# Kernel optimization log

Measured on AMD Instinct MI355X. Metric: run time of the kernel, lower is better.

Reference implementation:

```python
import jax, jax.numpy as jnp
import numpy as np

HIDDEN = 1024
Q_OUT = 2048
KV_OUT = 1024
HEAD_DIM = 128
N_Q = Q_OUT // HEAD_DIM      # 16
N_KV = KV_OUT // HEAD_DIM    # 8
EPS = 1e-6
ROPE_BASE = 10000.0


def _rms_norm(x, w, eps=EPS):
    # normalize over last dim (head_dim)
    ms = jnp.mean(x * x, axis=-1, keepdims=True)
    return x * jax.lax.rsqrt(ms + eps) * w


def _rope_cos_sin(t, dim=HEAD_DIM, base=ROPE_BASE):
    inv_freq = 1.0 / (base ** (jnp.arange(0, dim, 2, dtype=jnp.float32) / dim))
    pos = jnp.arange(t, dtype=jnp.float32)
    freqs = pos[:, None] * inv_freq[None, :]          # (T, D/2)
    emb = jnp.concatenate([freqs, freqs], axis=-1)    # (T, D)
    return jnp.cos(emb), jnp.sin(emb)


def _rotate_half(x):
    d = x.shape[-1] // 2
    return jnp.concatenate([-x[..., d:], x[..., :d]], axis=-1)


def setup_inputs() -> dict:
    key = jax.random.key(0)
    ks = jax.random.split(key, 7)
    def lin(k, fan_in, fan_out):
        # nn.Linear default init: U(-1/sqrt(fan_in), 1/sqrt(fan_in)); stored as (in, out) for x @ W
        bound = 1.0 / np.sqrt(fan_in)
        return jax.random.uniform(k, (fan_in, fan_out), jnp.float32, -bound, bound)
    return {
        "x": jax.random.normal(ks[0], (2, 2048, HIDDEN), jnp.float32),
        "Wq": lin(ks[1], HIDDEN, Q_OUT),
        "Wk": lin(ks[2], HIDDEN, KV_OUT),
        "Wv": lin(ks[3], HIDDEN, KV_OUT),
        "Wo": lin(ks[4], Q_OUT, HIDDEN),
        "q_norm_w": jnp.ones((HEAD_DIM,), jnp.float32),
        "k_norm_w": jnp.ones((HEAD_DIM,), jnp.float32),
    }


def reference(x, Wq, Wk, Wv, Wo, q_norm_w, k_norm_w):
    b, t, _ = x.shape
    # QKV projections, shaped to (B, H, T, D)
    q = (x @ Wq).reshape(b, t, N_Q, HEAD_DIM).transpose(0, 2, 1, 3)
    k = (x @ Wk).reshape(b, t, N_KV, HEAD_DIM).transpose(0, 2, 1, 3)
    v = (x @ Wv).reshape(b, t, N_KV, HEAD_DIM).transpose(0, 2, 1, 3)
    # per-head RMSNorm on q/k
    q = _rms_norm(q, q_norm_w)
    k = _rms_norm(k, k_norm_w)
    # RoPE (positions 0..T-1)
    cos, sin = _rope_cos_sin(t)                        # (T, D)
    cos = cos[None, None]; sin = sin[None, None]       # (1,1,T,D)
    q = q * cos + _rotate_half(q) * sin
    k = k * cos + _rotate_half(k) * sin
    # GQA: repeat_interleave kv heads to match q heads
    rep = N_Q // N_KV
    k_r = jnp.repeat(k, rep, axis=1)                   # (B, Hq, T, D)
    v_r = jnp.repeat(v, rep, axis=1)
    # causal attention
    scores = jnp.einsum('bhqd,bhkd->bhqk', q, k_r) / jnp.sqrt(jnp.asarray(HEAD_DIM, x.dtype))
    causal = jnp.triu(jnp.full((t, t), -jnp.inf, dtype=scores.dtype), k=1)[None, None]
    attn = jax.nn.softmax(scores + causal, axis=-1)
    out = jnp.einsum('bhqk,bhkd->bhqd', attn, v_r)     # (B, Hq, T, D)
    out = out.transpose(0, 2, 1, 3).reshape(b, t, Q_OUT)
    return out @ Wo
```

## Files before the change

### kernel.cpp

```cpp
#include <hip/hip_runtime.h>
#include <math.h>

typedef __attribute__((ext_vector_type(8))) short short8;
typedef __attribute__((ext_vector_type(4))) float f32x4;
typedef __attribute__((ext_vector_type(4))) unsigned int uint4v;

#define HIDDEN 1024
#define QOUT 2048
#define KVOUT 1024
#define HD 128
#define TSEQ 2048

__device__ __forceinline__ float bf2f(unsigned short h) {
    union { unsigned int u; float f; } x; x.u = ((unsigned int)h) << 16; return x.f;
}
__device__ __forceinline__ unsigned short f2bf(float f) {
    union { float f; unsigned int u; } x; x.f = f;
    unsigned int r = (x.u + 0x7fffu + ((x.u >> 16) & 1u)) >> 16;
    return (unsigned short)r;
}
__device__ __forceinline__ unsigned int cvtpk(float lo, float hi) {
    unsigned int r;
    asm("v_cvt_pk_bf16_f32 %0, %1, %2" : "=v"(r) : "v"(lo), "v"(hi));
    return r;
}
__device__ __forceinline__ void pl32(unsigned int& a, unsigned int& b) {
    asm("v_permlane32_swap_b32 %0, %1" : "+v"(a), "+v"(b));
}
__device__ __forceinline__ void pl16(unsigned int& a, unsigned int& b) {
    asm("v_permlane16_swap_b32 %0, %1" : "+v"(a), "+v"(b));
}

__device__ __forceinline__ void glds16(const unsigned short* g, unsigned short* l) {
    __builtin_amdgcn_global_load_lds(
        (const __attribute__((address_space(1))) unsigned int*)g,
        (__attribute__((address_space(3))) unsigned int*)l, 16, 0, 0);
}

__global__ __launch_bounds__(256) void prep(const float* __restrict__ x,
                                            const float* __restrict__ Wq,
                                            const float* __restrict__ Wk,
                                            const float* __restrict__ Wv,
                                            const float* __restrict__ Wo,
                                            unsigned short* __restrict__ xb,
                                            unsigned short* __restrict__ Wt,
                                            unsigned short* __restrict__ Wot) {
    int bid = blockIdx.x;
    int tid = threadIdx.x;
    if (bid < 4096) {
        int i = bid * 256 + tid;
        float4 v = *(const float4*)(x + (size_t)i * 4);
        unsigned short o[4] = {f2bf(v.x), f2bf(v.y), f2bf(v.z), f2bf(v.w)};
        *(unsigned long long*)(xb + (size_t)i * 4) = *(unsigned long long*)o;
        return;
    }
    bid -= 4096;
    const float* W; unsigned short* D; int K, N;
    if (bid < 512)       { W = Wq; D = Wt;                          K = 1024; N = 2048; }
    else if (bid < 768)  { bid -= 512;  W = Wk; D = Wt + (size_t)2048 * 1024; K = 1024; N = 1024; }
    else if (bid < 1024) { bid -= 768;  W = Wv; D = Wt + (size_t)3072 * 1024; K = 1024; N = 1024; }
    else                 { bid -= 1024; W = Wo; D = Wot;                      K = 2048; N = 1024; }
    __shared__ __attribute__((aligned(16))) unsigned short Ls[64 * 72];
    int ntiles = N >> 6;
    int kt = bid / ntiles, nt = bid - kt * ntiles;
    int k0 = kt * 64, n0 = nt * 64;
    for (int t = 0; t < 4; t++) {
        int idx = tid + t * 256;
        int r = idx >> 4, seg = idx & 15;
        float4 v = *(const float4*)(W + (size_t)(k0 + r) * N + n0 + seg * 4);
        int c = seg * 4;
        Ls[(c + 0) * 72 + r] = f2bf(v.x);
        Ls[(c + 1) * 72 + r] = f2bf(v.y);
        Ls[(c + 2) * 72 + r] = f2bf(v.z);
        Ls[(c + 3) * 72 + r] = f2bf(v.w);
    }
    __syncthreads();
    for (int t = 0; t < 2; t++) {
        int idx = tid + t * 256;
        int rr = idx >> 3, seg = idx & 7;
        uint4v v = *(const uint4v*)(Ls + rr * 72 + seg * 8);
        *(uint4v*)(D + (size_t)(n0 + rr) * K + k0 + seg * 8) = v;
    }
}

template <int OUT_BF16, int BN>
__global__ __launch_bounds__(256) void gemm_bt(const unsigned short* __restrict__ A,
                                               const unsigned short* __restrict__ Bt,
                                               void* __restrict__ Cout,
                                               int M, int N, int K) {
    constexpr int MT = (BN == 128) ? 4 : 2;
    __shared__ __attribute__((aligned(16))) unsigned short As[2][128 * 32];
    __shared__ __attribute__((aligned(16))) unsigned short Bs[2][BN * 32];
    const int tid = threadIdx.x;
    const int lane = tid & 63;
    const int warp = tid >> 6;
    const int ln = lane & 15;
    const int quad = lane >> 4;
    const int wm = (BN == 128) ? (warp >> 1) : warp;
    const int wn = (BN == 128) ? (warp & 1) : 0;
    const int m0 = blockIdx.y * 128;
    const int n0 = blockIdx.x * BN;

    const int srow = lane >> 2;
    const int schunk = (lane & 3) ^ (srow & 3);
    const unsigned short* Ag = A + (size_t)(m0 + warp * 16 + srow) * K + schunk * 8;
    const unsigned short* Bg = Bt + (size_t)(n0 + warp * 16 + srow) * K + schunk * 8;

    f32x4 acc[MT][4];
#pragma unroll
    for (int i = 0; i < MT; i++)
#pragma unroll
        for (int j = 0; j < 4; j++) acc[i][j] = (f32x4){0.f, 0.f, 0.f, 0.f};

    auto stage = [&](int k0, int bi) {
        glds16(Ag + k0, As[bi] + warp * 16 * 32);
        glds16(Ag + (size_t)64 * K + k0, As[bi] + warp * 16 * 32 + 64 * 32);
        glds16(Bg + k0, Bs[bi] + warp * 16 * 32);
        if (BN == 128) glds16(Bg + (size_t)64 * K + k0, Bs[bi] + warp * 16 * 32 + 64 * 32);
    };

    const int rq = quad ^ (ln & 3);
    const int KI = K >> 5;
    stage(0, 0);
    for (int it = 0; it < KI; it++) {
        __syncthreads();
        if (it + 1 < KI) stage((it + 1) << 5, (it + 1) & 1);
        const unsigned short* Ab = As[it & 1];
        const unsigned short* Bb = Bs[it & 1];
        short8 af[MT], bf[4];
#pragma unroll
        for (int mt = 0; mt < MT; mt++)
            af[mt] = *(const short8*)(Ab + (wm * (MT * 16) + mt * 16 + ln) * 32 + rq * 8);
#pragma unroll
        for (int nt = 0; nt < 4; nt++)
            bf[nt] = *(const short8*)(Bb + (wn * 64 + nt * 16 + ln) * 32 + rq * 8);
#pragma unroll
        for (int mt = 0; mt < MT; mt++)
#pragma unroll
            for (int nt = 0; nt < 4; nt++)
                acc[mt][nt] = __builtin_amdgcn_mfma_f32_16x16x32_bf16(bf[nt], af[mt], acc[mt][nt], 0, 0, 0);
    }
#pragma unroll
    for (int mt = 0; mt < MT; mt++) {
        int row = m0 + wm * (MT * 16) + mt * 16 + ln;
#pragma unroll
        for (int nt = 0; nt < 4; nt++) {
            int colb = n0 + wn * 64 + nt * 16 + quad * 4;
            if (OUT_BF16) {
                unsigned long long pk =
                    (unsigned long long)cvtpk(acc[mt][nt][0], acc[mt][nt][1]) |
                    ((unsigned long long)cvtpk(acc[mt][nt][2], acc[mt][nt][3]) << 32);
                *(unsigned long long*)((unsigned short*)Cout + (size_t)row * N + colb) = pk;
            } else {
                *(f32x4*)((float*)Cout + (size_t)row * N + colb) = acc[mt][nt];
            }
        }
    }
}

template <int OUT_BF16>
__global__ __launch_bounds__(256) void gemm_o(const unsigned short* __restrict__ A,
                                              const unsigned short* __restrict__ Bt,
                                              void* __restrict__ Cout,
                                              int M, int N, int K) {
    __shared__ __attribute__((aligned(16))) unsigned short As[2][128 * 64];
    __shared__ __attribute__((aligned(16))) unsigned short Bs[2][64 * 64];
    const int tid = threadIdx.x;
    const int lane = tid & 63;
    const int warp = tid >> 6;
    const int ln = lane & 15;
    const int quad = lane >> 4;
    const int m0 = blockIdx.y * 128;
    const int n0 = blockIdx.x * 64;

    const int srow = lane >> 3;
    const int schunk = (lane & 7) ^ srow;
    const unsigned short* Ag = A + (size_t)(m0 + warp * 32 + srow) * K + schunk * 8;
    const unsigned short* Bg = Bt + (size_t)(n0 + warp * 16 + srow) * K + schunk * 8;

    f32x4 acc[2][4];
#pragma unroll
    for (int i = 0; i < 2; i++)
#pragma unroll
        for (int j = 0; j < 4; j++) acc[i][j] = (f32x4){0.f, 0.f, 0.f, 0.f};

    auto stage = [&](int k0, int bi) {
#pragma unroll
        for (int g = 0; g < 4; g++)
            glds16(Ag + (size_t)(g * 8) * K + k0, As[bi] + (warp * 32 + g * 8) * 64);
#pragma unroll
        for (int g = 0; g < 2; g++)
            glds16(Bg + (size_t)(g * 8) * K + k0, Bs[bi] + (warp * 16 + g * 8) * 64);
    };

    const int KI = K >> 6;
    stage(0, 0);
    for (int it = 0; it < KI; it++) {
        __syncthreads();
        if (it + 1 < KI) stage((it + 1) << 6, (it + 1) & 1);
        const unsigned short* Ab = As[it & 1];
        const unsigned short* Bb = Bs[it & 1];
#pragma unroll
        for (int ks = 0; ks < 2; ks++) {
            const int rc = ((ks << 2) + quad) ^ (ln & 7);
            short8 af[2], bf[4];
#pragma unroll
            for (int mt = 0; mt < 2; mt++)
                af[mt] = *(const short8*)(Ab + (warp * 32 + mt * 16 + ln) * 64 + rc * 8);
#pragma unroll
            for (int nt = 0; nt < 4; nt++)
                bf[nt] = *(const short8*)(Bb + (nt * 16 + ln) * 64 + rc * 8);
#pragma unroll
            for (int mt = 0; mt < 2; mt++)
#pragma unroll
                for (int nt = 0; nt < 4; nt++)
                    acc[mt][nt] = __builtin_amdgcn_mfma_f32_16x16x32_bf16(bf[nt], af[mt], acc[mt][nt], 0, 0, 0);
        }
    }
#pragma unroll
    for (int mt = 0; mt < 2; mt++) {
        int row = m0 + warp * 32 + mt * 16 + ln;
#pragma unroll
        for (int nt = 0; nt < 4; nt++) {
            int colb = n0 + nt * 16 + quad * 4;
            if (OUT_BF16) {
                unsigned long long pk =
                    (unsigned long long)cvtpk(acc[mt][nt][0], acc[mt][nt][1]) |
                    ((unsigned long long)cvtpk(acc[mt][nt][2], acc[mt][nt][3]) << 32);
                *(unsigned long long*)((unsigned short*)Cout + (size_t)row * N + colb) = pk;
            } else {
                *(f32x4*)((float*)Cout + (size_t)row * N + colb) = acc[mt][nt];
            }
        }
    }
}

__global__ __launch_bounds__(256) void nrvt(const unsigned short* __restrict__ QKV,
                                            const float* __restrict__ qw,
                                            const float* __restrict__ kw,
                                            unsigned short* __restrict__ Q,
                                            unsigned short* __restrict__ Kb,
                                            unsigned short* __restrict__ Vt) {
    if (blockIdx.x < 12288) {
        const int tid = threadIdx.x;
        const int l5 = tid & 31;
        const int task = blockIdx.x * 8 + (tid >> 5);
        const int tok = task / 24;
        const int slot = task - tok * 24;
        const int b = tok >> 11, t = tok & 2047;
        const float* w;
        unsigned short* dst;
        int col0;
        float sc;
        if (slot < 16) {
            col0 = slot * HD;
            dst = Q + ((size_t)(b * 16 + slot) * TSEQ + t) * HD;
            w = qw;
            sc = 0.12750580997495268f;
        } else {
            int hk = slot - 16;
            col0 = QOUT + hk * HD;
            dst = Kb + ((size_t)(b * 8 + hk) * TSEQ + t) * HD;
            w = kw;
            sc = 1.0f;
        }
        const unsigned short* row = QKV + (size_t)tok * 4096 + col0;
        unsigned long long pkin = *(const unsigned long long*)(row + l5 * 4);
        unsigned short us[4];
        *(unsigned long long*)us = pkin;
        float e[4];
        float ss = 0.f;
#pragma unroll
        for (int k = 0; k < 4; k++) { e[k] = bf2f(us[k]); ss += e[k] * e[k]; }
#pragma unroll
        for (int off = 1; off < 32; off <<= 1) ss += __shfl_xor(ss, off);
        float rr = rsqrtf(ss * (1.0f / 128.0f) + 1e-6f);
        float4 wv = *(const float4*)(w + l5 * 4);
        float n[4] = { e[0] * rr * wv.x, e[1] * rr * wv.y, e[2] * rr * wv.z, e[3] * rr * wv.w };
        float np[4];
#pragma unroll
        for (int k = 0; k < 4; k++) np[k] = __shfl_xor(n[k], 16);
        const float tf = (float)t;
        const int fb = (l5 & 15) * 4;
        const bool hi = (l5 >= 16);
        unsigned short outs[4];
#pragma unroll
        for (int k = 0; k < 4; k++) {
            float invf = __builtin_exp2f(-(float)(fb + k) * 0.20762050593045951f);
            float sf, cf;
            __sincosf(tf * invf, &sf, &cf);
            float o = hi ? (n[k] * cf + np[k] * sf) : (n[k] * cf - np[k] * sf);
            outs[k] = f2bf(o * sc);
        }
        *(unsigned long long*)(dst + l5 * 4) = *(unsigned long long*)outs;
        return;
    }
    __shared__ __attribute__((aligned(16))) unsigned short Ls[128 * 72];
    int bid = blockIdx.x - 12288;
    int tt = bid & 31, hk = (bid >> 5) & 7, b = bid >> 8;
    int t0 = tt * 64;
    int tid = threadIdx.x;
    const unsigned short* base = QKV + (size_t)(b * 2048 + t0) * 4096 + 3072 + hk * 128;
    for (int i = 0; i < 4; i++) {
        int idx = tid + i * 256;
        int r = idx >> 4, seg = idx & 15;
        uint4v v = *(const uint4v*)(base + (size_t)r * 4096 + seg * 8);
        unsigned short* pv = (unsigned short*)&v;
        int d = seg * 8;
        for (int jj = 0; jj < 8; jj++) Ls[(d + jj) * 72 + r] = pv[jj];
    }
    __syncthreads();
    unsigned short* out = Vt + (size_t)(b * 8 + hk) * 128 * 2048;
    for (int i = 0; i < 4; i++) {
        int idx = tid + i * 256;
        int d = idx >> 3, seg = idx & 7;
        uint4v v = *(const uint4v*)(Ls + d * 72 + seg * 8);
        *(uint4v*)(out + (size_t)d * 2048 + t0 + seg * 8) = v;
    }
}

__global__ __launch_bounds__(512, 4) void attn(const unsigned short* __restrict__ Q,
                                               const unsigned short* __restrict__ Kg,
                                               const unsigned short* __restrict__ Vt,
                                               unsigned short* __restrict__ Og) {
    __shared__ __attribute__((aligned(16))) unsigned short Ks[2][64 * 128];
    __shared__ __attribute__((aligned(16))) unsigned short Vs[2][128 * 64];
    const int p = blockIdx.x;
    const int bh = blockIdx.y;
    const int b = bh >> 4, h = bh & 15, hk = h >> 1;
    const int tid = threadIdx.x;
    const int w = tid >> 6, lane = tid & 63, ln = lane & 15, quad = lane >> 4;
    const int sg = w >> 2;
    const int wi = w & 3;
    const int tile = sg ? (31 - p) : p;
    const int jdiag = tile;
    const int qrow0 = tile * 64 + wi * 16;

    const unsigned short* Kbase = Kg + (size_t)(b * 8 + hk) * TSEQ * HD;
    const unsigned short* Vbase = Vt + (size_t)(b * 8 + hk) * HD * TSEQ;
    const unsigned short* Qh = Q + (size_t)(b * 16 + h) * TSEQ * HD;

    short8 qf[4];
#pragma unroll
    for (int kt = 0; kt < 4; kt++)
        qf[kt] = *(const short8*)(Qh + (size_t)(qrow0 + ln) * HD + kt * 32 + quad * 8);

    f32x4 o[8];
    f32x4 lac = (f32x4){0.f, 0.f, 0.f, 0.f};
#pragma unroll
    for (int ot = 0; ot < 8; ot++) o[ot] = (f32x4){0.f, 0.f, 0.f, 0.f};
    float m_ = -1e30f;

    const int kr = lane >> 4;
    const int kc = lane & 15;
    const int vr = lane >> 3;
    const int vc = lane & 7;

    auto stage_kv = [&](int jt, int bi) {
        const int j0s = jt * 64;
        unsigned short* KsB = Ks[bi];
        unsigned short* VsB = Vs[bi];
#pragma unroll
        for (int c = 0; c < 2; c++) {
            int row = w * 8 + c * 4 + kr;
            glds16(Kbase + (size_t)(j0s + row) * HD + ((kc ^ (row & 15)) * 8),
                   KsB + (w * 8 + c * 4) * 128);
        }
#pragma unroll
        for (int c = 0; c < 2; c++) {
            int d = w * 16 + c * 8 + vr;
            glds16(Vbase + (size_t)d * TSEQ + j0s + ((vc ^ (d & 7)) * 8),
                   VsB + (w * 16 + c * 8) * 64);
        }
    };

    short8 ones8;
#pragma unroll
    for (int i = 0; i < 8; i++) ones8[i] = (short)0x3F80;

    const int nT = 32 - p;
    stage_kv(0, 0);
    for (int j = 0; j < nT; j++) {
        __syncthreads();
        if (j + 1 < nT) stage_kv(j + 1, (j + 1) & 1);
        const unsigned short* KsC = Ks[j & 1];
        const unsigned short* VsC = Vs[j & 1];
        const bool act = sg ? true : (j <= jdiag);
        if (act) {
            f32x4 s[4];
#pragma unroll
            for (int kb = 0; kb < 4; kb++) s[kb] = (f32x4){0.f, 0.f, 0.f, 0.f};
            __builtin_amdgcn_s_setprio(1);
#pragma unroll
            for (int kt = 0; kt < 4; kt++) {
                short8 kf[4];
#pragma unroll
                for (int kb = 0; kb < 4; kb++)
                    kf[kb] = *(const short8*)(KsC + (kb * 16 + ln) * 128 + (((kt * 4 + quad) ^ ln) * 8));
#pragma unroll
                for (int kb = 0; kb < 4; kb++)
                    s[kb] = __builtin_amdgcn_mfma_f32_16x16x32_bf16(kf[kb], qf[kt], s[kb], 0, 0, 0);
            }
            __builtin_amdgcn_s_setprio(0);
            float mk[4];
            if (j == jdiag) {
                const int qloc = wi * 16 + ln;
#pragma unroll
                for (int kb = 0; kb < 4; kb++) {
#pragma unroll
                    for (int r = 0; r < 4; r++) {
                        int kvloc = kb * 16 + quad * 4 + r;
                        if (kvloc > qloc) s[kb][r] = -1e30f;
                    }
                    mk[kb] = fmaxf(fmaxf(s[kb][0], s[kb][1]), fmaxf(s[kb][2], s[kb][3]));
                }
            } else {
#pragma unroll
                for (int kb = 0; kb < 4; kb++)
                    mk[kb] = fmaxf(fmaxf(s[kb][0], s[kb][1]), fmaxf(s[kb][2], s[kb][3]));
            }
            float mx = fmaxf(fmaxf(mk[0], mk[1]), fmaxf(mk[2], mk[3]));
            float mn = m_;
            bool needR = false;
            float alpha = 1.f;
            if (!__all(mx <= mn + 8.0f)) {
                mx = fmaxf(mx, __shfl_xor(mx, 16));
                mx = fmaxf(mx, __shfl_xor(mx, 32));
                mn = fmaxf(m_, mx);
                alpha = __builtin_exp2f(m_ - mn);
                m_ = mn;
                needR = true;
            }
            unsigned int u[8];
#pragma unroll
            for (int kb = 0; kb < 4; kb++) {
                float p0 = __builtin_exp2f(s[kb][0] - mn);
                float p1 = __builtin_exp2f(s[kb][1] - mn);
                float p2 = __builtin_exp2f(s[kb][2] - mn);
                float p3 = __builtin_exp2f(s[kb][3] - mn);
                u[kb * 2 + 0] = cvtpk(p0, p1);
                u[kb * 2 + 1] = cvtpk(p2, p3);
            }
            pl32(u[0], u[2]); pl16(u[0], u[2]);
            pl32(u[1], u[3]); pl16(u[1], u[3]);
            pl32(u[4], u[6]); pl16(u[4], u[6]);
            pl32(u[5], u[7]); pl16(u[5], u[7]);
            union { unsigned int uu[4]; short8 s8; } P0, P1;
            P0.uu[0] = u[0]; P0.uu[1] = u[1]; P0.uu[2] = u[2]; P0.uu[3] = u[3];
            P1.uu[0] = u[4]; P1.uu[1] = u[5]; P1.uu[2] = u[6]; P1.uu[3] = u[7];
            short8 pf0 = P0.s8;
            short8 pf1 = P1.s8;
            if (needR) {
#pragma unroll
                for (int ot = 0; ot < 8; ot++)
#pragma unroll
                    for (int r = 0; r < 4; r++) o[ot][r] *= alpha;
#pragma unroll
                for (int r = 0; r < 4; r++) lac[r] *= alpha;
            }
            __builtin_amdgcn_s_setprio(1);
            lac = __builtin_amdgcn_mfma_f32_16x16x32_bf16(ones8, pf0, lac, 0, 0, 0);
            lac = __builtin_amdgcn_mfma_f32_16x16x32_bf16(ones8, pf1, lac, 0, 0, 0);
#pragma unroll
            for (int ot = 0; ot < 8; ot++) {
                short8 vf0 = *(const short8*)(VsC + (ot * 16 + ln) * 64 + ((quad ^ (ln & 7)) * 8));
                short8 vf1 = *(const short8*)(VsC + (ot * 16 + ln) * 64 + (((4 + quad) ^ (ln & 7)) * 8));
                o[ot] = __builtin_amdgcn_mfma_f32_16x16x32_bf16(vf0, pf0, o[ot], 0, 0, 0);
                o[ot] = __builtin_amdgcn_mfma_f32_16x16x32_bf16(vf1, pf1, o[ot], 0, 0, 0);
            }
            __builtin_amdgcn_s_setprio(0);
        }
    }
    float inv = 1.0f / lac[0];
    size_t rowoff = ((size_t)(b * TSEQ + qrow0 + ln)) * QOUT + h * 128 + quad * 4;
#pragma unroll
    for (int ot = 0; ot < 8; ot++) {
        unsigned long long pk =
            (unsigned long long)cvtpk(o[ot][0] * inv, o[ot][1] * inv) |
            ((unsigned long long)cvtpk(o[ot][2] * inv, o[ot][3] * inv) << 32);
        *(unsigned long long*)(Og + rowoff + ot * 16) = pk;
    }
}

extern "C" void kernel_launch(void* const* d_in, const int* in_sizes, int n_in,
                              void* d_out, int out_size, void* d_ws, size_t ws_size,
                              hipStream_t stream) {
    (void)in_sizes; (void)n_in; (void)out_size;
    const float* x  = (const float*)d_in[0];
    const float* Wq = (const float*)d_in[1];
    const float* Wk = (const float*)d_in[2];
    const float* Wv = (const float*)d_in[3];
    const float* Wo = (const float*)d_in[4];
    const float* qw = (const float*)d_in[5];
    const float* kw = (const float*)d_in[6];

    char* ws = (char*)d_ws;
    const size_t MB = 1024 * 1024;
    unsigned short* Wt   = (unsigned short*)(ws);
    unsigned short* Wot  = (unsigned short*)(ws + 8 * MB);
    unsigned short* QKVb = (unsigned short*)(ws + 12 * MB);
    unsigned short* xb   = (unsigned short*)(ws + 44 * MB);
    unsigned short* Qb   = (unsigned short*)(ws + 52 * MB);
    unsigned short* Kb   = (unsigned short*)(ws + 68 * MB);
    unsigned short* Vtb  = (unsigned short*)(ws + 76 * MB);
    unsigned short* Ob   = (unsigned short*)(ws + 84 * MB);
    if (ws_size < 100 * MB) return;

    prep<<<dim3(5632), 256, 0, stream>>>(x, Wq, Wk, Wv, Wo, xb, Wt, Wot);
    gemm_bt<1, 128><<<dim3(32, 32), 256, 0, stream>>>(xb, Wt, QKVb, 4096, 4096, 1024);
    nrvt<<<dim3(12800), 256, 0, stream>>>(QKVb, qw, kw, Qb, Kb, Vtb);
    attn<<<dim3(16, 32), 512, 0, stream>>>(Qb, Kb, Vtb, Ob);
    gemm_o<0><<<dim3(16, 32), 256, 0, stream>>>(Ob, Wot, (float*)d_out, 4096, 1024, 2048);
}
```

Before: 251.3 us.

## Halve attention KV tile to 32 keys and double occupancy bound

Shrinks the per-iteration KV tile in the flash-attention kernel from 64 to 32 keys, halving LDS use, and raises launch bounds from 4 to 8 blocks per CU. The V tile gets a new packed layout with two head-dim rows per LDS row, and the causal diagonal is tracked per 32-key half-tile, so warps skip more fully masked work. The intent is more resident blocks and finer causal skipping. The cost is twice as many barriers and staging rounds per query tile, and tighter register limits that could cause spills.

```diff
diff --git a/kernel.cpp b/kernel.cpp
--- a/kernel.cpp
+++ b/kernel.cpp
@@ -319,12 +319,12 @@
     }
 }
 
-__global__ __launch_bounds__(512, 4) void attn(const unsigned short* __restrict__ Q,
+__global__ __launch_bounds__(512, 8) void attn(const unsigned short* __restrict__ Q,
                                                const unsigned short* __restrict__ Kg,
                                                const unsigned short* __restrict__ Vt,
                                                unsigned short* __restrict__ Og) {
-    __shared__ __attribute__((aligned(16))) unsigned short Ks[2][64 * 128];
-    __shared__ __attribute__((aligned(16))) unsigned short Vs[2][128 * 64];
+    __shared__ __attribute__((aligned(16))) unsigned short Ks[2][32 * 128];
+    __shared__ __attribute__((aligned(16))) unsigned short Vs[2][64 * 64];
     const int p = blockIdx.x;
     const int bh = blockIdx.y;
     const int b = bh >> 4, h = bh & 15, hk = h >> 1;
@@ -333,7 +333,7 @@
     const int sg = w >> 2;
     const int wi = w & 3;
     const int tile = sg ? (31 - p) : p;
-    const int jdiag = tile;
+    const int jdiag = 2 * tile + (wi >> 1);
     const int qrow0 = tile * 64 + wi * 16;
 
     const unsigned short* Kbase = Kg + (size_t)(b * 8 + hk) * TSEQ * HD;
@@ -351,26 +351,19 @@
     for (int ot = 0; ot < 8; ot++) o[ot] = (f32x4){0.f, 0.f, 0.f, 0.f};
     float m_ = -1e30f;
 
-    const int kr = lane >> 4;
-    const int kc = lane & 15;
-    const int vr = lane >> 3;
-    const int vc = lane & 7;
-
     auto stage_kv = [&](int jt, int bi) {
-        const int j0s = jt * 64;
-        unsigned short* KsB = Ks[bi];
-        unsigned short* VsB = Vs[bi];
-#pragma unroll
-        for (int c = 0; c < 2; c++) {
-            int row = w * 8 + c * 4 + kr;
-            glds16(Kbase + (size_t)(j0s + row) * HD + ((kc ^ (row & 15)) * 8),
-                   KsB + (w * 8 + c * 4) * 128);
-        }
-#pragma unroll
-        for (int c = 0; c < 2; c++) {
-            int d = w * 16 + c * 8 + vr;
-            glds16(Vbase + (size_t)d * TSEQ + j0s + ((vc ^ (d & 7)) * 8),
-                   VsB + (w * 16 + c * 8) * 64);
+        const int j0s = jt * 32;
+        {
+            int row = w * 4 + (lane >> 4);
+            int kchunk = lane & 15;
+            glds16(Kbase + (size_t)(j0s + row) * HD + ((kchunk ^ (row & 15)) * 8),
+                   Ks[bi] + (w * 4) * 128);
+        }
+        {
+            int r = w * 8 + (lane >> 3);
+            int c = (lane & 7) ^ (r & 7);
+            glds16(Vbase + (size_t)(2 * r + (c >> 2)) * TSEQ + j0s + (c & 3) * 8,
+                   Vs[bi] + (w * 8) * 64);
         }
     };
 
@@ -378,48 +371,42 @@
 #pragma unroll
     for (int i = 0; i < 8; i++) ones8[i] = (short)0x3F80;
 
-    const int nT = 32 - p;
+    const int nT = 64 - 2 * p;
     stage_kv(0, 0);
     for (int j = 0; j < nT; j++) {
         __syncthreads();
         if (j + 1 < nT) stage_kv(j + 1, (j + 1) & 1);
         const unsigned short* KsC = Ks[j & 1];
         const unsigned short* VsC = Vs[j & 1];
-        const bool act = sg ? true : (j <= jdiag);
-        if (act) {
-            f32x4 s[4];
-#pragma unroll
-            for (int kb = 0; kb < 4; kb++) s[kb] = (f32x4){0.f, 0.f, 0.f, 0.f};
+        if (j <= jdiag) {
+            f32x4 s[2];
+            s[0] = (f32x4){0.f, 0.f, 0.f, 0.f};
+            s[1] = (f32x4){0.f, 0.f, 0.f, 0.f};
             __builtin_amdgcn_s_setprio(1);
 #pragma unroll
             for (int kt = 0; kt < 4; kt++) {
-                short8 kf[4];
-#pragma unroll
-                for (int kb = 0; kb < 4; kb++)
+                short8 kf[2];
+#pragma unroll
+                for (int kb = 0; kb < 2; kb++)
                     kf[kb] = *(const short8*)(KsC + (kb * 16 + ln) * 128 + (((kt * 4 + quad) ^ ln) * 8));
 #pragma unroll
-                for (int kb = 0; kb < 4; kb++)
+                for (int kb = 0; kb < 2; kb++)
                     s[kb] = __builtin_amdgcn_mfma_f32_16x16x32_bf16(kf[kb], qf[kt], s[kb], 0, 0, 0);
             }
             __builtin_amdgcn_s_setprio(0);
-            float mk[4];
             if (j == jdiag) {
-                const int qloc = wi * 16 + ln;
-#pragma unroll
-                for (int kb = 0; kb < 4; kb++) {
+                const int qrel = wi * 16 + ln - ((wi >> 1) << 5);
+#pragma unroll
+                for (int kb = 0; kb < 2; kb++)
 #pragma unroll
                     for (int r = 0; r < 4; r++) {
-                        int kvloc = kb * 16 + quad * 4 + r;
-                        if (kvloc > qloc) s[kb][r] = -1e30f;
+                        int kvl = kb * 16 + quad * 4 + r;
+                        if (kvl > qrel) s[kb][r] = -1e30f;
                     }
-                    mk[kb] = fmaxf(fmaxf(s[kb][0], s[kb][1]), fmaxf(s[kb][2], s[kb][3]));
-                }
-            } else {
-#pragma unroll
-                for (int kb = 0; kb < 4; kb++)
-                    mk[kb] = fmaxf(fmaxf(s[kb][0], s[kb][1]), fmaxf(s[kb][2], s[kb][3]));
-            }
-            float mx = fmaxf(fmaxf(mk[0], mk[1]), fmaxf(mk[2], mk[3]));
+            }
+            float mk0 = fmaxf(fmaxf(s[0][0], s[0][1]), fmaxf(s[0][2], s[0][3]));
+            float mk1 = fmaxf(fmaxf(s[1][0], s[1][1]), fmaxf(s[1][2], s[1][3]));
+            float mx = fmaxf(mk0, mk1);
             float mn = m_;
             bool needR = false;
             float alpha = 1.f;
@@ -431,9 +418,9 @@
                 m_ = mn;
                 needR = true;
             }
-            unsigned int u[8];
-#pragma unroll
-            for (int kb = 0; kb < 4; kb++) {
+            unsigned int u[4];
+#pragma unroll
+            for (int kb = 0; kb < 2; kb++) {
                 float p0 = __builtin_exp2f(s[kb][0] - mn);
                 float p1 = __builtin_exp2f(s[kb][1] - mn);
                 float p2 = __builtin_exp2f(s[kb][2] - mn);
@@ -443,13 +430,9 @@
             }
             pl32(u[0], u[2]); pl16(u[0], u[2]);
             pl32(u[1], u[3]); pl16(u[1], u[3]);
-            pl32(u[4], u[6]); pl16(u[4], u[6]);
-            pl32(u[5], u[7]); pl16(u[5], u[7]);
-            union { unsigned int uu[4]; short8 s8; } P0, P1;
+            union { unsigned int uu[4]; short8 s8; } P0;
             P0.uu[0] = u[0]; P0.uu[1] = u[1]; P0.uu[2] = u[2]; P0.uu[3] = u[3];
-            P1.uu[0] = u[4]; P1.uu[1] = u[5]; P1.uu[2] = u[6]; P1.uu[3] = u[7];
-            short8 pf0 = P0.s8;
-            short8 pf1 = P1.s8;
+            short8 pf = P0.s8;
             if (needR) {
 #pragma unroll
                 for (int ot = 0; ot < 8; ot++)
@@ -459,14 +442,13 @@
                 for (int r = 0; r < 4; r++) lac[r] *= alpha;
             }
             __builtin_amdgcn_s_setprio(1);
-            lac = __builtin_amdgcn_mfma_f32_16x16x32_bf16(ones8, pf0, lac, 0, 0, 0);
-            lac = __builtin_amdgcn_mfma_f32_16x16x32_bf16(ones8, pf1, lac, 0, 0, 0);
+            lac = __builtin_amdgcn_mfma_f32_16x16x32_bf16(ones8, pf, lac, 0, 0, 0);
 #pragma unroll
             for (int ot = 0; ot < 8; ot++) {
-                short8 vf0 = *(const short8*)(VsC + (ot * 16 + ln) * 64 + ((quad ^ (ln & 7)) * 8));
-                short8 vf1 = *(const short8*)(VsC + (ot * 16 + ln) * 64 + (((4 + quad) ^ (ln & 7)) * 8));
-                o[ot] = __builtin_amdgcn_mfma_f32_16x16x32_bf16(vf0, pf0, o[ot], 0, 0, 0);
-                o[ot] = __builtin_amdgcn_mfma_f32_16x16x32_bf16(vf1, pf1, o[ot], 0, 0, 0);
+                int vrow = ot * 8 + (ln >> 1);
+                int cc = (((ln & 1) << 2) + quad) ^ (vrow & 7);
+                short8 vf = *(const short8*)(VsC + vrow * 64 + cc * 8);
+                o[ot] = __builtin_amdgcn_mfma_f32_16x16x32_bf16(vf, pf, o[ot], 0, 0, 0);
             }
             __builtin_amdgcn_s_setprio(0);
         }
```

New measurement: 443.0 us. +76.3%, slower.
